# Kernel optimization log

Measured on AMD Instinct MI355X. Metric: run time of the kernel, lower is better.

Reference implementation:

```python
import jax, jax.numpy as jnp
from jax import lax
import numpy as np

NUM_HEADS = 16
NUM_HEADS_KV = 4
HEAD_DIM = 128
D_CONV = 4
ROT_DIM = 128
ROT_BASE = 10000.0
CAUSAL = True


def setup_inputs() -> dict:
    key = jax.random.key(0)
    ks = jax.random.split(key, 7)
    B, S, E = 2, 2048, 2048
    QKV = HEAD_DIM * (NUM_HEADS + 2 * NUM_HEADS_KV)  # 3072
    return {
        "x": jax.random.normal(ks[0], (B, S, E), jnp.float32),
        "W_in": jax.random.normal(ks[1], (QKV, E), jnp.float32) * 0.02,
        "b_in": jax.random.normal(ks[2], (QKV,), jnp.float32) * 0.02,
        "conv_w": jax.random.normal(ks[3], (QKV, D_CONV), jnp.float32) * 0.1,
        "conv_b": jax.random.normal(ks[4], (QKV,), jnp.float32) * 0.02,
        "W_out": jax.random.normal(ks[5], (E, NUM_HEADS * HEAD_DIM), jnp.float32) * 0.02,
        "b_out": jax.random.normal(ks[6], (E,), jnp.float32) * 0.02,
    }


def _rotary(x, cos, sin):
    # x: [B,S,H,D], non-interleaved rotary over first ROT_DIM dims (here full D)
    x1, x2 = x[..., : ROT_DIM // 2], x[..., ROT_DIM // 2 : ROT_DIM]
    c = cos[None, :, None, :]
    s = sin[None, :, None, :]
    rot = jnp.concatenate([x1 * c - x2 * s, x2 * c + x1 * s], axis=-1)
    return jnp.concatenate([rot, x[..., ROT_DIM:]], axis=-1)


def reference(x, W_in, b_in, conv_w, conv_b, W_out, b_out):
    B, S, E = x.shape
    QKV = conv_w.shape[0]
    # fused in-projection
    qkv = jnp.einsum("bse,fe->bsf", x, W_in) + b_in  # [B,S,QKV]
    # depthwise causal conv1d (left pad d_conv-1, equivalent to torch pad+trim)
    qkv_t = jnp.transpose(qkv, (0, 2, 1))  # [B,C,S]
    qkv_t = jnp.pad(qkv_t, ((0, 0), (0, 0), (D_CONV - 1, 0)))
    conv = lax.conv_general_dilated(
        qkv_t, conv_w[:, None, :], window_strides=(1,), padding="VALID",
        feature_group_count=QKV, dimension_numbers=("NCH", "OIH", "NCH"))
    qkv = jnp.transpose(conv + conv_b[None, :, None], (0, 2, 1))  # [B,S,QKV]
    # split q / kv
    q_dim = NUM_HEADS * HEAD_DIM
    q = qkv[..., :q_dim].reshape(B, S, NUM_HEADS, HEAD_DIM)
    kv = qkv[..., q_dim:].reshape(B, S, 2, NUM_HEADS_KV, HEAD_DIM)
    k, v = kv[:, :, 0], kv[:, :, 1]
    # rotary embedding on q and k
    t = jnp.arange(S, dtype=jnp.float32)
    inv_freq = 1.0 / (ROT_BASE ** (jnp.arange(0, ROT_DIM, 2, dtype=jnp.float32) / ROT_DIM))
    freqs = t[:, None] * inv_freq[None, :]  # [S, ROT_DIM/2]
    cos, sin = jnp.cos(freqs), jnp.sin(freqs)
    q = _rotary(q, cos, sin)
    k = _rotary(k, cos, sin)
    # GQA: repeat kv heads
    rep = NUM_HEADS // NUM_HEADS_KV
    k = jnp.repeat(k, rep, axis=2)  # [B,S,H,D]
    v = jnp.repeat(v, rep, axis=2)
    scale = 1.0 / jnp.sqrt(jnp.float32(HEAD_DIM))
    scores = jnp.einsum("bshd,bthd->bhst", q, k) * scale  # [B,H,S,S]
    if CAUSAL:
        mask = jnp.tril(jnp.ones((S, S), dtype=bool))
        scores = jnp.where(mask[None, None], scores, jnp.finfo(scores.dtype).min)
    attn = jax.nn.softmax(scores, axis=-1)
    ctx = jnp.einsum("bhst,bthd->bshd", attn, v).reshape(B, S, q_dim)
    return jnp.einsum("bsf,ef->bse", ctx, W_out) + b_out
```

## Files before the change

### kernel.cpp

```cpp
#include <hip/hip_runtime.h>
#include <hip/hip_bf16.h>

#define B_   2
#define S_   2048
#define E_   2048
#define QKV_ 3072
#define NH   16
#define NKV  4
#define HD   128
#define SL   16

typedef __attribute__((ext_vector_type(8))) short bf16x8;
typedef __attribute__((ext_vector_type(4))) float f32x4;
typedef unsigned short u16;
typedef unsigned int   u32;

__device__ __forceinline__ float bf2f(u16 u) {
  union { u32 i; float f; } v; v.i = ((u32)u) << 16; return v.f;
}
__device__ __forceinline__ u16 f2bf(float f) {
  union { float f; u32 u; } v; v.f = f;
  return (u16)((v.u + 0x7FFFu + ((v.u >> 16) & 1u)) >> 16);
}
__device__ __forceinline__ u32 pkbf(float a, float b) {
  __hip_bfloat162 h = __float22bfloat162_rn(float2{a, b});
  u32 r; __builtin_memcpy(&r, &h, 4); return r;
}
__device__ __forceinline__ float ex2(float x) { return __builtin_amdgcn_exp2f(x); }
__device__ __forceinline__ void load_lds16(const u16* g, u16* l) {
  __builtin_amdgcn_global_load_lds((const __attribute__((address_space(1))) void*)g,
                                   (__attribute__((address_space(3))) void*)l, 16, 0, 0);
}

__global__ __launch_bounds__(256) void f2b_conv(const float* __restrict__ in,
                                                u16* __restrict__ out, int n4) {
  const int i = blockIdx.x * 256 + threadIdx.x;
  if (i >= n4) return;
  const float4 v = ((const float4*)in)[i];
  ushort4 o;
  o.x = f2bf(v.x); o.y = f2bf(v.y); o.z = f2bf(v.z); o.w = f2bf(v.w);
  ((ushort4*)out)[i] = o;
}

__global__ __launch_bounds__(256) void rope_tab(float* __restrict__ c,
                                                float* __restrict__ s) {
  const int idx = blockIdx.x * 256 + threadIdx.x;
  const int t = idx >> 6, i = idx & 63;
  const float invf = powf(10000.0f, -(float)i * (1.0f / 64.0f));
  float sn, cs;
  sincosf((float)t * invf, &sn, &cs);
  c[idx] = cs; s[idx] = sn;
}

template <int OUT_BF16>
__global__ __launch_bounds__(512, 2) void gemm256(const u16* __restrict__ A,
                                                  const u16* __restrict__ Bm,
                                                  const float* __restrict__ bias,
                                                  void* __restrict__ C,
                                                  int M, int N, int K) {
  __shared__ u16 sm[2][2][256 * 64];
  const int tid = threadIdx.x;
  const int lane = tid & 63;
  const int wave = tid >> 6;
  const int wm = wave >> 2, wn = wave & 3;
  const int L15 = lane & 15, Lq = lane >> 4;
  const int m0 = blockIdx.y * 256, n0 = blockIdx.x * 256;
  const int NT = K >> 6;

  const int srow = tid >> 3;
  const int sdst = (tid & 7) * 8;
  const int ssrc = ((tid & 7) ^ (srow & 7)) * 8;

  auto stageA = [&](int T, int h, int j) {
    const int row = h * 128 + j * 64 + srow;
    load_lds16(A + (size_t)(m0 + row) * K + T * 64 + ssrc,
               &sm[T & 1][0][row * 64 + sdst]);
  };
  auto stageB = [&](int T, int h, int j) {
    const int row = h * 128 + j * 64 + srow;
    load_lds16(Bm + (size_t)(n0 + row) * K + T * 64 + ssrc,
               &sm[T & 1][1][row * 64 + sdst]);
  };
  auto rdA = [&](int p, int ms, int mf, int kk) -> bf16x8 {
    const int row = wm * 128 + ms * 64 + mf * 16 + L15;
    const int u = (kk * 4 + Lq) ^ (row & 7);
    return *(const bf16x8*)&sm[p][0][row * 64 + u * 8];
  };
  auto rdB = [&](int p, int ns, int nf, int kk) -> bf16x8 {
    const int row = wn * 64 + ns * 32 + nf * 16 + L15;
    const int u = (kk * 4 + Lq) ^ (row & 7);
    return *(const bf16x8*)&sm[p][1][row * 64 + u * 8];
  };

  f32x4 acc[8][4] = {};

  stageA(0, 0, 0); stageA(0, 0, 1);
  stageB(0, 0, 0); stageB(0, 0, 1);
  stageA(0, 1, 0); stageA(0, 1, 1);
  stageB(0, 1, 0); stageB(0, 1, 1);
  stageB(1, 0, 0); stageB(1, 0, 1);
  stageA(1, 0, 0); stageA(1, 0, 1);
  asm volatile("s_waitcnt vmcnt(4)" ::: "memory");
  asm volatile("s_barrier" ::: "memory");

  bf16x8 af[4][2], bf0[2][2], bf1[2][2];

#define MFMA_QUAD(MS, NS, BF)                                                     \
  __builtin_amdgcn_s_setprio(1);                                                  \
  __builtin_amdgcn_sched_barrier(0);                                              \
  _Pragma("unroll")                                                               \
  for (int kk = 0; kk < 2; ++kk)                                                  \
    _Pragma("unroll")                                                             \
    for (int mf = 0; mf < 4; ++mf)                                                \
      _Pragma("unroll")                                                           \
      for (int nf = 0; nf < 2; ++nf)                                              \
        acc[MS * 4 + mf][NS * 2 + nf] = __builtin_amdgcn_mfma_f32_16x16x32_bf16(  \
            af[mf][kk], BF[nf][kk], acc[MS * 4 + mf][NS * 2 + nf], 0, 0, 0);      \
  __builtin_amdgcn_sched_barrier(0);                                              \
  __builtin_amdgcn_s_setprio(0);

  for (int T = 0; T < NT; ++T) {
    const int p = T & 1;
#pragma unroll
    for (int mf = 0; mf < 4; ++mf)
#pragma unroll
      for (int kk = 0; kk < 2; ++kk) af[mf][kk] = rdA(p, 0, mf, kk);
#pragma unroll
    for (int nf = 0; nf < 2; ++nf)
#pragma unroll
      for (int kk = 0; kk < 2; ++kk) bf0[nf][kk] = rdB(p, 0, nf, kk);
    if (T + 1 < NT) { stageA(T + 1, 1, 0); stageA(T + 1, 1, 1); }
    asm volatile("s_barrier" ::: "memory");
    MFMA_QUAD(0, 0, bf0)
    asm volatile("s_barrier" ::: "memory");
#pragma unroll
    for (int nf = 0; nf < 2; ++nf)
#pragma unroll
      for (int kk = 0; kk < 2; ++kk) bf1[nf][kk] = rdB(p, 1, nf, kk);
    if (T + 1 < NT) { stageB(T + 1, 1, 0); stageB(T + 1, 1, 1); }
    asm volatile("s_barrier" ::: "memory");
    MFMA_QUAD(0, 1, bf1)
    asm volatile("s_barrier" ::: "memory");
#pragma unroll
    for (int mf = 0; mf < 4; ++mf)
#pragma unroll
      for (int kk = 0; kk < 2; ++kk) af[mf][kk] = rdA(p, 1, mf, kk);
    if (T + 2 < NT) { stageB(T + 2, 0, 0); stageB(T + 2, 0, 1); }
    asm volatile("s_barrier" ::: "memory");
    MFMA_QUAD(1, 0, bf0)
    asm volatile("s_barrier" ::: "memory");
    if (T + 2 < NT) {
      stageA(T + 2, 0, 0); stageA(T + 2, 0, 1);
      asm volatile("s_waitcnt vmcnt(4)" ::: "memory");
    } else {
      asm volatile("s_waitcnt vmcnt(0)" ::: "memory");
    }
    asm volatile("s_barrier" ::: "memory");
    MFMA_QUAD(1, 1, bf1)
    asm volatile("s_barrier" ::: "memory");
  }
#undef MFMA_QUAD

#pragma unroll
  for (int ms = 0; ms < 2; ++ms)
#pragma unroll
    for (int mf = 0; mf < 4; ++mf) {
      const int grow0 = m0 + wm * 128 + ms * 64 + mf * 16 + Lq * 4;
#pragma unroll
      for (int ns = 0; ns < 2; ++ns)
#pragma unroll
        for (int nf = 0; nf < 2; ++nf) {
          const int gcol = n0 + wn * 64 + ns * 32 + nf * 16 + L15;
          const float bv = bias[gcol];
          const f32x4 v = acc[ms * 4 + mf][ns * 2 + nf];
#pragma unroll
          for (int r = 0; r < 4; ++r) {
            const float o = v[r] + bv;
            if (OUT_BF16) ((u16*)C)[(size_t)(grow0 + r) * N + gcol] = f2bf(o);
            else          ((float*)C)[(size_t)(grow0 + r) * N + gcol] = o;
          }
        }
    }
}

__global__ __launch_bounds__(256) void conv_rope(const u16* __restrict__ qkv,
                                                 const float* __restrict__ cw,
                                                 const float* __restrict__ cb,
                                                 const float* __restrict__ ct,
                                                 const float* __restrict__ st,
                                                 u16* __restrict__ qo,
                                                 u16* __restrict__ ko,
                                                 u16* __restrict__ vtmp) {
  const int blk = blockIdx.x;
  const int b = blk >> 7;
  const int s0 = (blk & 127) * SL;
  const u16* qb = qkv + (size_t)b * S_ * QKV_;

  for (int u = threadIdx.x; u < 896; u += 256) {
    if (u < 640) {
      const int hs = u >> 5, ip = u & 31, i = ip * 2;
      int f1; u16* outbase; float scale;
      if (hs < 16) {
        f1 = hs * HD + i;
        outbase = qo + (size_t)(b * NH + hs) * S_ * HD;
        scale = 0.08838834764831845f * 1.4426950408889634f;
      } else {
        f1 = NH * HD + (hs - 16) * HD + i;
        outbase = ko + (size_t)(b * NKV + (hs - 16)) * S_ * HD;
        scale = 1.0f;
      }
      const int f2 = f1 + 64;
      const float4 wA0 = *(const float4*)&cw[f1 * 4];
      const float4 wA1 = *(const float4*)&cw[(f1 + 1) * 4];
      const float4 wB0 = *(const float4*)&cw[f2 * 4];
      const float4 wB1 = *(const float4*)&cw[(f2 + 1) * 4];
      const float cA0 = cb[f1], cA1 = cb[f1 + 1], cB0 = cb[f2], cB1 = cb[f2 + 1];
      float A0[3], A1[3], B0[3], B1[3];
#pragma unroll
      for (int j = 0; j < 3; ++j) {
        const int t = s0 - 3 + j;
        if (t >= 0) {
          const u32 pa = *(const u32*)&qb[(size_t)t * QKV_ + f1];
          const u32 pb = *(const u32*)&qb[(size_t)t * QKV_ + f2];
          A0[j] = bf2f((u16)pa); A1[j] = bf2f((u16)(pa >> 16));
          B0[j] = bf2f((u16)pb); B1[j] = bf2f((u16)(pb >> 16));
        } else { A0[j] = A1[j] = B0[j] = B1[j] = 0.f; }
      }
      for (int s = s0; s < s0 + SL; ++s) {
        const u32 pa = *(const u32*)&qb[(size_t)s * QKV_ + f1];
        const u32 pb = *(const u32*)&qb[(size_t)s * QKV_ + f2];
        const float nA0 = bf2f((u16)pa), nA1 = bf2f((u16)(pa >> 16));
        const float nB0 = bf2f((u16)pb), nB1 = bf2f((u16)(pb >> 16));
        const float x1a = cA0 + wA0.x * A0[0] + wA0.y * A0[1] + wA0.z * A0[2] + wA0.w * nA0;
        const float x1b = cA1 + wA1.x * A1[0] + wA1.y * A1[1] + wA1.z * A1[2] + wA1.w * nA1;
        const float x2a = cB0 + wB0.x * B0[0] + wB0.y * B0[1] + wB0.z * B0[2] + wB0.w * nB0;
        const float x2b = cB1 + wB1.x * B1[0] + wB1.y * B1[1] + wB1.z * B1[2] + wB1.w * nB1;
        const float2 cs = *(const float2*)&ct[s * 64 + i];
        const float2 sn = *(const float2*)&st[s * 64 + i];
        u16* outp = outbase + (size_t)s * HD;
        *(u32*)&outp[i]      = pkbf((x1a * cs.x - x2a * sn.x) * scale,
                                    (x1b * cs.y - x2b * sn.y) * scale);
        *(u32*)&outp[i + 64] = pkbf((x2a * cs.x + x1a * sn.x) * scale,
                                    (x2b * cs.y + x1b * sn.y) * scale);
        A0[0] = A0[1]; A0[1] = A0[2]; A0[2] = nA0;
        A1[0] = A1[1]; A1[1] = A1[2]; A1[2] = nA1;
        B0[0] = B0[1]; B0[1] = B0[2]; B0[2] = nB0;
        B1[0] = B1[1]; B1[1] = B1[2]; B1[2] = nB1;
      }
    } else {
      const int vu = u - 640, h = vu >> 6, d = (vu & 63) * 2;
      const int f = (NH + NKV) * HD + h * HD + d;
      const float4 w0 = *(const float4*)&cw[f * 4];
      const float4 w1 = *(const float4*)&cw[(f + 1) * 4];
      const float c0 = cb[f], c1 = cb[f + 1];
      float V0[3], V1[3];
#pragma unroll
      for (int j = 0; j < 3; ++j) {
        const int t = s0 - 3 + j;
        if (t >= 0) {
          const u32 p = *(const u32*)&qb[(size_t)t * QKV_ + f];
          V0[j] = bf2f((u16)p); V1[j] = bf2f((u16)(p >> 16));
        } else { V0[j] = V1[j] = 0.f; }
      }
      u16* vrow = vtmp + (size_t)(b * NKV + h) * S_ * HD + d;
      for (int s = s0; s < s0 + SL; ++s) {
        const u32 p = *(const u32*)&qb[(size_t)s * QKV_ + f];
        const float n0 = bf2f((u16)p), n1 = bf2f((u16)(p >> 16));
        const float v0 = c0 + w0.x * V0[0] + w0.y * V0[1] + w0.z * V0[2] + w0.w * n0;
        const float v1 = c1 + w1.x * V1[0] + w1.y * V1[1] + w1.z * V1[2] + w1.w * n1;
        *(u32*)&vrow[(size_t)s * HD] = pkbf(v0, v1);
        V0[0] = V0[1]; V0[1] = V0[2]; V0[2] = n0;
        V1[0] = V1[1]; V1[1] = V1[2]; V1[2] = n1;
      }
    }
  }
}

__global__ __launch_bounds__(256) void vtrans(const u16* __restrict__ vin,
                                              u16* __restrict__ vout) {
  __shared__ u16 t[64][72];
  const int bh = blockIdx.z;
  const int d0 = blockIdx.y * 64;
  const int s0 = blockIdx.x * 64;
  const u16* ip = vin + ((size_t)bh * S_ + s0) * HD + d0;
  const int r = threadIdx.x >> 4, c4 = (threadIdx.x & 15) * 4;
#pragma unroll
  for (int j = 0; j < 4; ++j) {
    const ushort4 v = *(const ushort4*)&ip[(size_t)(r + j * 16) * HD + c4];
    t[c4 + 0][r + j * 16] = v.x;
    t[c4 + 1][r + j * 16] = v.y;
    t[c4 + 2][r + j * 16] = v.z;
    t[c4 + 3][r + j * 16] = v.w;
  }
  __syncthreads();
  const int dl = threadIdx.x >> 2, sc = (threadIdx.x & 3) * 16;
  u16* op = vout + (size_t)bh * HD * S_ + (size_t)(d0 + dl) * S_ + s0 + sc;
  *(bf16x8*)op       = *(const bf16x8*)&t[dl][sc];
  *(bf16x8*)(op + 8) = *(const bf16x8*)&t[dl][sc + 8];
}

__global__ __launch_bounds__(256, 2) void attn(const u16* __restrict__ q,
                                               const u16* __restrict__ k,
                                               const u16* __restrict__ v,
                                               u16* __restrict__ ctx) {
  __shared__ u16 Ks[2][64 * 128];
  __shared__ u16 Vs[128 * 64];
  __shared__ u16 P[4][16 * 64];
  const int tid = threadIdx.x, wave = tid >> 6, lane = tid & 63;
  const int L15 = lane & 15, Lq = lane >> 4;
  const int bh = blockIdx.y;
  const int b = bh >> 4, h = bh & 15, hk = h >> 2;

  const u16* kb = k + (size_t)(b * NKV + hk) * S_ * HD;
  const u16* vb = v + (size_t)(b * NKV + hk) * HD * S_;

  const int rx = L15 & 7;
  int koff[4], voff[2], poff[2];
#pragma unroll
  for (int c = 0; c < 4; ++c) koff[c] = ((c * 4 + Lq) ^ rx) * 8;
#pragma unroll
  for (int kc = 0; kc < 2; ++kc) {
    voff[kc] = ((kc * 4 + Lq) ^ rx) * 8;
    poff[kc] = L15 * 64 + ((kc * 4 + Lq) ^ rx) * 8;
  }

  const int ksl = tid >> 4, kcp = tid & 15;
  const int vsl = tid >> 3, vcp = tid & 7;

  for (int pass = 0; pass < 2; ++pass) {
    const int qt = pass ? (31 - blockIdx.x) : blockIdx.x;
    const int q0 = qt * 64;
    const int base = q0 + wave * 16;

    bf16x8 qf[4];
    {
      const u16* qp = q + ((size_t)bh * S_ + base + L15) * HD + Lq * 8;
#pragma unroll
      for (int c = 0; c < 4; ++c) qf[c] = *(const bf16x8*)(qp + c * 32);
    }

    f32x4 acc[8] = {};
    float m_i[4], l_i[4];
#pragma unroll
    for (int r = 0; r < 4; ++r) { m_i[r] = -1e30f; l_i[r] = 0.f; }

    const int ktmax = qt + 1;

#pragma unroll
    for (int j = 0; j < 4; ++j) {
      const int krow = j * 16 + ksl;
      load_lds16(kb + (size_t)krow * HD + (kcp ^ (krow & 7)) * 8,
                 &Ks[0][(krow * 16 + kcp) * 8]);
      const int vrow = j * 32 + vsl;
      load_lds16(vb + (size_t)vrow * S_ + (vcp ^ (vrow & 7)) * 8,
                 &Vs[(vrow * 8 + vcp) * 8]);
    }
    __syncthreads();

    for (int kt = 0; kt < ktmax; ++kt) {
      const int k0 = kt * 64;
      const int cur = kt & 1;
      if (kt > 0) {
#pragma unroll
        for (int j = 0; j < 4; ++j) {
          const int vrow = j * 32 + vsl;
          load_lds16(vb + (size_t)vrow * S_ + k0 + (vcp ^ (vrow & 7)) * 8,
                     &Vs[(vrow * 8 + vcp) * 8]);
        }
      }
      if (kt + 1 < ktmax) {
        const int kn = k0 + 64;
#pragma unroll
        for (int j = 0; j < 4; ++j) {
          const int krow = j * 16 + ksl;
          load_lds16(kb + (size_t)(kn + krow) * HD + (kcp ^ (krow & 7)) * 8,
                     &Ks[cur ^ 1][(krow * 16 + kcp) * 8]);
        }
      }
      f32x4 sc[4];
#pragma unroll
      for (int nt = 0; nt < 4; ++nt) sc[nt] = f32x4{0.f, 0.f, 0.f, 0.f};
#pragma unroll
      for (int nt = 0; nt < 4; ++nt) {
#pragma unroll
        for (int c = 0; c < 4; ++c) {
          const bf16x8 kf = *(const bf16x8*)&Ks[cur][(nt * 16 + L15) * 128 + koff[c]];
          sc[nt] = __builtin_amdgcn_mfma_f32_16x16x32_bf16(qf[c], kf, sc[nt], 0, 0, 0);
        }
      }
      if (k0 + 63 > base) {
#pragma unroll
        for (int nt = 0; nt < 4; ++nt) {
          const int col = k0 + nt * 16 + L15;
#pragma unroll
          for (int r = 0; r < 4; ++r) {
            const int row = base + Lq * 4 + r;
            if (col > row) sc[nt][r] = -1e30f;
          }
        }
      }
      float mloc[4];
      bool nm = false;
#pragma unroll
      for (int r = 0; r < 4; ++r) {
        float m = fmaxf(fmaxf(sc[0][r], sc[1][r]), fmaxf(sc[2][r], sc[3][r]));
        m = fmaxf(m, __shfl_xor(m, 1));
        m = fmaxf(m, __shfl_xor(m, 2));
        m = fmaxf(m, __shfl_xor(m, 4));
        m = fmaxf(m, __shfl_xor(m, 8));
        mloc[r] = m;
        nm |= (m > m_i[r]);
      }
      const bool anynew = (__ballot(nm) != 0ull);
      float rsum[4];
      {
        float mnew[4];
#pragma unroll
        for (int r = 0; r < 4; ++r) {
          mnew[r] = anynew ? fmaxf(m_i[r], mloc[r]) : m_i[r];
          rsum[r] = 0.f;
        }
        float pv[4][4];
#pragma unroll
        for (int nt = 0; nt < 4; ++nt)
#pragma unroll
          for (int r = 0; r < 4; ++r) {
            pv[nt][r] = ex2(sc[nt][r] - mnew[r]);
            rsum[r] += pv[nt][r];
          }
#pragma unroll
        for (int nt = 0; nt < 4; ++nt) {
          const int cch = nt * 2 + (L15 >> 3), clo = L15 & 7;
#pragma unroll
          for (int rp = 0; rp < 2; ++rp) {
            const u32 pk = pkbf(pv[nt][rp * 2], pv[nt][rp * 2 + 1]);
            const int row0 = Lq * 4 + rp * 2;
            P[wave][row0 * 64 + (((cch ^ (row0 & 7)) << 3) | clo)] = (u16)pk;
            const int row1 = row0 + 1;
            P[wave][row1 * 64 + (((cch ^ (row1 & 7)) << 3) | clo)] = (u16)(pk >> 16);
          }
        }
        if (anynew) {
          float alpha[4];
#pragma unroll
          for (int r = 0; r < 4; ++r) {
            alpha[r] = ex2(m_i[r] - mnew[r]);
            m_i[r] = mnew[r];
          }
#pragma unroll
          for (int dt = 0; dt < 8; ++dt)
#pragma unroll
            for (int r = 0; r < 4; ++r) acc[dt][r] *= alpha[r];
#pragma unroll
          for (int r = 0; r < 4; ++r) l_i[r] *= alpha[r];
        }
      }
#pragma unroll
      for (int r = 0; r < 4; ++r) {
        float s = rsum[r];
        s += __shfl_xor(s, 1);
        s += __shfl_xor(s, 2);
        s += __shfl_xor(s, 4);
        s += __shfl_xor(s, 8);
        l_i[r] += s;
      }
      __syncthreads();
      {
        bf16x8 pa[2];
#pragma unroll
        for (int kc = 0; kc < 2; ++kc)
          pa[kc] = *(const bf16x8*)&P[wave][poff[kc]];
#pragma unroll
        for (int dt = 0; dt < 8; ++dt)
#pragma unroll
          for (int kc = 0; kc < 2; ++kc) {
            const bf16x8 vf = *(const bf16x8*)&Vs[(dt * 16 + L15) * 64 + voff[kc]];
            acc[dt] = __builtin_amdgcn_mfma_f32_16x16x32_bf16(pa[kc], vf, acc[dt], 0, 0, 0);
          }
      }
      __syncthreads();
    }
    {
      float inv[4];
#pragma unroll
      for (int r = 0; r < 4; ++r) inv[r] = 1.f / l_i[r];
      u16* cp = ctx + ((size_t)b * S_ + base) * (NH * HD) + h * HD;
#pragma unroll
      for (int dt = 0; dt < 8; ++dt)
#pragma unroll
        for (int rp = 0; rp < 2; ++rp) {
          const u32 pk = pkbf(acc[dt][rp * 2] * inv[rp * 2],
                              acc[dt][rp * 2 + 1] * inv[rp * 2 + 1]);
          cp[(size_t)(Lq * 4 + rp * 2) * (NH * HD) + dt * 16 + L15] = (u16)pk;
          cp[(size_t)(Lq * 4 + rp * 2 + 1) * (NH * HD) + dt * 16 + L15] = (u16)(pk >> 16);
        }
    }
  }
}

extern "C" void kernel_launch(void* const* d_in, const int* in_sizes, int n_in,
                              void* d_out, int out_size, void* d_ws, size_t ws_size,
                              hipStream_t stream) {
  const float* x     = (const float*)d_in[0];
  const float* W_in  = (const float*)d_in[1];
  const float* b_in  = (const float*)d_in[2];
  const float* cw    = (const float*)d_in[3];
  const float* cb    = (const float*)d_in[4];
  const float* W_out = (const float*)d_in[5];
  const float* b_out = (const float*)d_in[6];

  char* ws = (char*)d_ws;
  u16* xb   = (u16*)(ws);
  u16* wib  = (u16*)(ws + 16777216);
  u16* wob  = (u16*)(ws + 29360128);
  u16* qkv  = (u16*)(ws + 37748736);
  u16* q_ws = (u16*)(ws + 62914560);
  u16* k_ws = (u16*)(ws + 79691776);
  u16* vt_ws= (u16*)(ws + 83886080);
  float* ctab = (float*)ws;
  float* stab = (float*)(ws + 524288);
  u16* vtmp = wib;
  u16* ctx  = xb;

  const int nx = B_ * S_ * E_ / 4, nwi = QKV_ * E_ / 4, nwo = E_ * NH * HD / 4;
  f2b_conv<<<dim3((nx  + 255) / 256), 256, 0, stream>>>(x,     xb,  nx);
  f2b_conv<<<dim3((nwi + 255) / 256), 256, 0, stream>>>(W_in,  wib, nwi);
  f2b_conv<<<dim3((nwo + 255) / 256), 256, 0, stream>>>(W_out, wob, nwo);

  gemm256<1><<<dim3(QKV_ / 256, (B_ * S_) / 256), 512, 0, stream>>>(
      xb, wib, b_in, (void*)qkv, B_ * S_, QKV_, E_);
  rope_tab<<<dim3(S_ * 64 / 256), 256, 0, stream>>>(ctab, stab);
  conv_rope<<<dim3(B_ * (S_ / SL)), 256, 0, stream>>>(qkv, cw, cb, ctab, stab, q_ws, k_ws, vtmp);
  vtrans<<<dim3(S_ / 64, HD / 64, B_ * NKV), 256, 0, stream>>>(vtmp, vt_ws);
  attn<<<dim3(16, B_ * NH), 256, 0, stream>>>(q_ws, k_ws, vt_ws, ctx);
  gemm256<0><<<dim3(E_ / 256, (B_ * S_) / 256), 512, 0, stream>>>(
      ctx, wob, b_out, d_out, B_ * S_, E_, NH * HD);
}
```

Before: 356.3 us.

## Add 256x128 tile GEMM for output projection and relax scheduling barriers

```diff
diff --git a/kernel.cpp b/kernel.cpp
--- a/kernel.cpp
+++ b/kernel.cpp
@@ -101,13 +101,12 @@
   stageB(1, 0, 0); stageB(1, 0, 1);
   stageA(1, 0, 0); stageA(1, 0, 1);
   asm volatile("s_waitcnt vmcnt(4)" ::: "memory");
-  asm volatile("s_barrier" ::: "memory");
+  __builtin_amdgcn_s_barrier();
 
   bf16x8 af[4][2], bf0[2][2], bf1[2][2];
 
 #define MFMA_QUAD(MS, NS, BF)                                                     \
   __builtin_amdgcn_s_setprio(1);                                                  \
-  __builtin_amdgcn_sched_barrier(0);                                              \
   _Pragma("unroll")                                                               \
   for (int kk = 0; kk < 2; ++kk)                                                  \
     _Pragma("unroll")                                                             \
@@ -116,7 +115,6 @@
       for (int nf = 0; nf < 2; ++nf)                                              \
         acc[MS * 4 + mf][NS * 2 + nf] = __builtin_amdgcn_mfma_f32_16x16x32_bf16(  \
             af[mf][kk], BF[nf][kk], acc[MS * 4 + mf][NS * 2 + nf], 0, 0, 0);      \
-  __builtin_amdgcn_sched_barrier(0);                                              \
   __builtin_amdgcn_s_setprio(0);
 
   for (int T = 0; T < NT; ++T) {
@@ -130,34 +128,34 @@
 #pragma unroll
       for (int kk = 0; kk < 2; ++kk) bf0[nf][kk] = rdB(p, 0, nf, kk);
     if (T + 1 < NT) { stageA(T + 1, 1, 0); stageA(T + 1, 1, 1); }
-    asm volatile("s_barrier" ::: "memory");
+    __builtin_amdgcn_s_barrier();
     MFMA_QUAD(0, 0, bf0)
-    asm volatile("s_barrier" ::: "memory");
+    __builtin_amdgcn_s_barrier();
 #pragma unroll
     for (int nf = 0; nf < 2; ++nf)
 #pragma unroll
       for (int kk = 0; kk < 2; ++kk) bf1[nf][kk] = rdB(p, 1, nf, kk);
     if (T + 1 < NT) { stageB(T + 1, 1, 0); stageB(T + 1, 1, 1); }
-    asm volatile("s_barrier" ::: "memory");
+    __builtin_amdgcn_s_barrier();
     MFMA_QUAD(0, 1, bf1)
-    asm volatile("s_barrier" ::: "memory");
+    __builtin_amdgcn_s_barrier();
 #pragma unroll
     for (int mf = 0; mf < 4; ++mf)
 #pragma unroll
       for (int kk = 0; kk < 2; ++kk) af[mf][kk] = rdA(p, 1, mf, kk);
     if (T + 2 < NT) { stageB(T + 2, 0, 0); stageB(T + 2, 0, 1); }
-    asm volatile("s_barrier" ::: "memory");
+    __builtin_amdgcn_s_barrier();
     MFMA_QUAD(1, 0, bf0)
-    asm volatile("s_barrier" ::: "memory");
+    __builtin_amdgcn_s_barrier();
     if (T + 2 < NT) {
       stageA(T + 2, 0, 0); stageA(T + 2, 0, 1);
       asm volatile("s_waitcnt vmcnt(4)" ::: "memory");
     } else {
       asm volatile("s_waitcnt vmcnt(0)" ::: "memory");
     }
-    asm volatile("s_barrier" ::: "memory");
+    __builtin_amdgcn_s_barrier();
     MFMA_QUAD(1, 1, bf1)
-    asm volatile("s_barrier" ::: "memory");
+    __builtin_amdgcn_s_barrier();
   }
 #undef MFMA_QUAD
 
@@ -181,6 +179,93 @@
           }
         }
     }
+}
+
+__global__ __launch_bounds__(512, 2) void gemm_n128(const u16* __restrict__ A,
+                                                    const u16* __restrict__ Bm,
+                                                    const float* __restrict__ bias,
+                                                    float* __restrict__ C,
+                                                    int M, int N, int K) {
+  __shared__ u16 sm[2][24576];
+  const int tid = threadIdx.x, lane = tid & 63, wave = tid >> 6;
+  const int wm = wave >> 1, wn = wave & 1;
+  const int L15 = lane & 15, Lq = lane >> 4;
+  const int m0 = blockIdx.y * 256, n0 = blockIdx.x * 128;
+  const int NT = K >> 6;
+
+  const int srow = tid >> 3;
+  const int sdst = (tid & 7) * 8;
+  const int ssrc = ((tid & 7) ^ (srow & 7)) * 8;
+
+  auto stage6 = [&](int T) {
+#pragma unroll
+    for (int c = 0; c < 4; ++c) {
+      const int row = c * 64 + srow;
+      load_lds16(A + (size_t)(m0 + row) * K + T * 64 + ssrc,
+                 &sm[T & 1][row * 64 + sdst]);
+    }
+#pragma unroll
+    for (int c = 0; c < 2; ++c) {
+      const int row = c * 64 + srow;
+      load_lds16(Bm + (size_t)(n0 + row) * K + T * 64 + ssrc,
+                 &sm[T & 1][16384 + row * 64 + sdst]);
+    }
+  };
+
+  f32x4 acc[4][4] = {};
+  stage6(0);
+
+  for (int T = 0; T < NT; ++T) {
+    const int p = T & 1;
+    if (T + 1 < NT) {
+      stage6(T + 1);
+      asm volatile("s_waitcnt vmcnt(6)" ::: "memory");
+    } else {
+      asm volatile("s_waitcnt vmcnt(0)" ::: "memory");
+    }
+    __builtin_amdgcn_s_barrier();
+    bf16x8 af[4][2], bfr[4][2];
+#pragma unroll
+    for (int mf = 0; mf < 4; ++mf)
+#pragma unroll
+      for (int kk = 0; kk < 2; ++kk) {
+        const int row = wm * 64 + mf * 16 + L15;
+        const int u = (kk * 4 + Lq) ^ (row & 7);
+        af[mf][kk] = *(const bf16x8*)&sm[p][row * 64 + u * 8];
+      }
+#pragma unroll
+    for (int nf = 0; nf < 4; ++nf)
+#pragma unroll
+      for (int kk = 0; kk < 2; ++kk) {
+        const int row = wn * 64 + nf * 16 + L15;
+        const int u = (kk * 4 + Lq) ^ (row & 7);
+        bfr[nf][kk] = *(const bf16x8*)&sm[p][16384 + row * 64 + u * 8];
+      }
+    __builtin_amdgcn_s_setprio(1);
+#pragma unroll
+    for (int kk = 0; kk < 2; ++kk)
+#pragma unroll
+      for (int mf = 0; mf < 4; ++mf)
+#pragma unroll
+        for (int nf = 0; nf < 4; ++nf)
+          acc[mf][nf] = __builtin_amdgcn_mfma_f32_16x16x32_bf16(
+              af[mf][kk], bfr[nf][kk], acc[mf][nf], 0, 0, 0);
+    __builtin_amdgcn_s_setprio(0);
+    __builtin_amdgcn_s_barrier();
+  }
+
+#pragma unroll
+  for (int mf = 0; mf < 4; ++mf) {
+    const int grow0 = m0 + wm * 64 + mf * 16 + Lq * 4;
+#pragma unroll
+    for (int nf = 0; nf < 4; ++nf) {
+      const int gcol = n0 + wn * 64 + nf * 16 + L15;
+      const float bv = bias[gcol];
+#pragma unroll
+      for (int r = 0; r < 4; ++r)
+        C[(size_t)(grow0 + r) * N + gcol] = acc[mf][nf][r] + bv;
+    }
+  }
 }
 
 __global__ __launch_bounds__(256) void conv_rope(const u16* __restrict__ qkv,
@@ -533,6 +618,6 @@
   conv_rope<<<dim3(B_ * (S_ / SL)), 256, 0, stream>>>(qkv, cw, cb, ctab, stab, q_ws, k_ws, vtmp);
   vtrans<<<dim3(S_ / 64, HD / 64, B_ * NKV), 256, 0, stream>>>(vtmp, vt_ws);
   attn<<<dim3(16, B_ * NH), 256, 0, stream>>>(q_ws, k_ws, vt_ws, ctx);
-  gemm256<0><<<dim3(E_ / 256, (B_ * S_) / 256), 512, 0, stream>>>(
-      ctx, wob, b_out, d_out, B_ * S_, E_, NH * HD);
-}
+  gemm_n128<<<dim3(E_ / 128, (B_ * S_) / 256), 512, 0, stream>>>(
+      ctx, wob, b_out, (float*)d_out, B_ * S_, E_, NH * HD);
+}
```

New measurement: 343.0 us. 3.7% less time.
